# Optimization experiments

Hardware: AMD Instinct MI355X
Metric: run time of the kernel (lower is better)

Reference implementation:

```python
import jax, jax.numpy as jnp
import numpy as np

D_MODEL = 1024
N_HEADS = 16
HEAD_DIM = 64  # 'hidden' per head; n_heads*hidden == d_model


def setup_inputs() -> dict:
    key = jax.random.key(0)
    ks = jax.random.split(key, 11)
    B, S = 4, 2048
    scale = 1.0 / np.sqrt(D_MODEL)
    return {
        "query": jax.random.normal(ks[0], (B, S, D_MODEL), jnp.float32),
        "key": jax.random.normal(ks[1], (B, S, D_MODEL), jnp.float32),
        "value": jax.random.normal(ks[2], (B, S, D_MODEL), jnp.float32),
        "Wq": jax.random.normal(ks[3], (D_MODEL, N_HEADS * HEAD_DIM), jnp.float32) * scale,
        "bq": jnp.zeros((N_HEADS * HEAD_DIM,), jnp.float32),
        "Wk": jax.random.normal(ks[4], (D_MODEL, N_HEADS * HEAD_DIM), jnp.float32) * scale,
        "bk": jnp.zeros((N_HEADS * HEAD_DIM,), jnp.float32),
        "Wv": jax.random.normal(ks[5], (D_MODEL, N_HEADS * HEAD_DIM), jnp.float32) * scale,
        "bv": jnp.zeros((N_HEADS * HEAD_DIM,), jnp.float32),
        "Wo": jax.random.normal(ks[6], (N_HEADS * HEAD_DIM, D_MODEL), jnp.float32) * scale,
        "bo": jnp.zeros((D_MODEL,), jnp.float32),
    }


def reference(query, key, value, Wq, bq, Wk, bk, Wv, bv, Wo, bo):
    B, Sq, _ = query.shape
    Sk = key.shape[1]
    # QKV projections -> [B, H, S, d]
    q = (query @ Wq + bq).reshape(B, Sq, N_HEADS, HEAD_DIM).transpose(0, 2, 1, 3)
    k = (key @ Wk + bk).reshape(B, Sk, N_HEADS, HEAD_DIM).transpose(0, 2, 1, 3)
    v = (value @ Wv + bv).reshape(B, Sk, N_HEADS, HEAD_DIM).transpose(0, 2, 1, 3)
    # scores [B, H, Sq, Sk]
    scores = jnp.einsum("bhqd,bhkd->bhqk", q, k) / np.sqrt(HEAD_DIM).astype(np.float32)
    probs = jax.nn.softmax(scores, axis=-1)  # dropout: identity (eval mode)
    z = jnp.einsum("bhqk,bhkd->bhqd", probs, v)
    z = z.transpose(0, 2, 1, 3).reshape(B, Sq, N_HEADS * HEAD_DIM)
    return z @ Wo + bo
```

## Files before the change

kernel.cpp:

```cpp
#include <hip/hip_runtime.h>
#include <hip/hip_bf16.h>

typedef unsigned short ushort_t;
typedef unsigned int u32;
typedef __attribute__((ext_vector_type(8))) short short8;
typedef short8 __attribute__((may_alias)) short8_ma;
typedef __attribute__((ext_vector_type(4))) float f32x4;
typedef f32x4 __attribute__((may_alias)) f32x4_ma;
typedef __attribute__((ext_vector_type(2))) unsigned int u32x2;
typedef u32x2 __attribute__((may_alias)) u32x2_ma;
typedef __attribute__((ext_vector_type(4))) unsigned int u32x4;
typedef u32x4 __attribute__((may_alias)) u32x4_ma;

#if __has_builtin(__builtin_amdgcn_exp2f)
#define EXP2(x) __builtin_amdgcn_exp2f(x)
#else
#define EXP2(x) exp2f(x)
#endif

__device__ __forceinline__ unsigned short f2bf(float f) {
    union { float f; unsigned int i; } x; x.f = f;
    unsigned int r = x.i + 0x7FFFu + ((x.i >> 16) & 1u);
    return (unsigned short)(r >> 16);
}
__device__ __forceinline__ unsigned int bfround(float f) {
    union { float f; unsigned int i; } x; x.f = f;
    return x.i + 0x7FFFu + ((x.i >> 16) & 1u);
}
__device__ __forceinline__ unsigned int pack2bf(float lo, float hi) {
    return __builtin_amdgcn_perm(bfround(hi), bfround(lo), 0x07060302u);
}
__device__ __forceinline__ u32 cvtpk_bf16(float lo, float hi) {
    u32 r;
    asm("v_cvt_pk_bf16_f32 %0, %1, %2" : "=v"(r) : "v"(lo), "v"(hi));
    return r;
}
__device__ __forceinline__ f32x4 mfma16x16x32(short8 a, short8 b, f32x4 c) {
    return __builtin_amdgcn_mfma_f32_16x16x32_bf16(a, b, c, 0, 0, 0);
}
typedef const __attribute__((address_space(1))) u32 gu32;
typedef __attribute__((address_space(3))) u32 lu32;
__device__ __forceinline__ void async16(const ushort_t* g, ushort_t* l) {
    __builtin_amdgcn_global_load_lds((gu32*)g, (lu32*)l, 16, 0, 0);
}

__global__ __launch_bounds__(256)
void cast3(const float* __restrict__ A0, const float* __restrict__ A1,
           const float* __restrict__ A2, ushort_t* __restrict__ O0,
           ushort_t* __restrict__ O1, ushort_t* __restrict__ O2) {
    const float* A; ushort_t* O;
    switch (blockIdx.z) {
        case 0: A = A0; O = O0; break;
        case 1: A = A1; O = O1; break;
        default: A = A2; O = O2; break;
    }
    size_t idx = ((size_t)blockIdx.x * 256 + threadIdx.x) * 8;
    f32x4 v0 = *(const f32x4_ma*)(A + idx);
    f32x4 v1 = *(const f32x4_ma*)(A + idx + 4);
    u32x4 pk;
    pk[0] = pack2bf(v0[0], v0[1]);
    pk[1] = pack2bf(v0[2], v0[3]);
    pk[2] = pack2bf(v1[0], v1[1]);
    pk[3] = pack2bf(v1[2], v1[3]);
    *(u32x4_ma*)(O + idx) = pk;
}

__global__ __launch_bounds__(256)
void transpose4(const float* __restrict__ W0, const float* __restrict__ W1,
                const float* __restrict__ W2, const float* __restrict__ W3,
                ushort_t* __restrict__ T0, ushort_t* __restrict__ T1,
                ushort_t* __restrict__ T2, ushort_t* __restrict__ T3) {
    __shared__ ushort_t tile[64][65];
    const float* W; ushort_t* T;
    switch (blockIdx.z) {
        case 0: W = W0; T = T0; break;
        case 1: W = W1; T = T1; break;
        case 2: W = W2; T = T2; break;
        default: W = W3; T = T3; break;
    }
    int bx = blockIdx.x * 64, by = blockIdx.y * 64;
    int tx = threadIdx.x & 63, ty = threadIdx.x >> 6;
    #pragma unroll
    for (int i = 0; i < 64; i += 4)
        tile[ty + i][tx] = f2bf(W[(size_t)(by + ty + i) * 1024 + bx + tx]);
    __syncthreads();
    #pragma unroll
    for (int i = 0; i < 64; i += 4)
        T[(size_t)(bx + ty + i) * 1024 + by + tx] = tile[tx][ty + i];
}

template<int MODE>
__global__ __launch_bounds__(256)
void gemm_async(const ushort_t* __restrict__ A, const ushort_t* __restrict__ Bt,
                const float* __restrict__ bias, void* __restrict__ Cab,
                int M, int N, int K, float outscale) {
    __shared__ __align__(16) ushort_t As[2][128 * 64];
    __shared__ __align__(16) ushort_t Bs[2][128 * 64];
    const int t = threadIdx.x;
    const int old = blockIdx.x + (blockIdx.y << 3);
    const int neu = ((old & 7) << 6) | (old >> 3);
    const int n0 = (neu & 7) * 128, m0 = (neu >> 3) * 128;
    const int w = t >> 6, lane = t & 63, quad = lane >> 4, lr = lane & 15;
    const int wm = (w >> 1) * 64, wn = (w & 1) * 64;
    const int lrow8 = lane >> 3, lchunk = lane & 7;
    const int sw = (lchunk ^ lrow8) * 8;

    f32x4 acc[4][4] = {};

    #define STAGEAB(dst, koff) do { \
        _Pragma("unroll") \
        for (int i_ = 0; i_ < 4; i_++) { \
            int ra_ = 32 * w + 8 * i_ + lrow8; \
            async16(A  + (size_t)(m0 + ra_) * K + (koff) + sw, &As[dst][(32 * w + 8 * i_) * 64]); \
            async16(Bt + (size_t)(n0 + ra_) * K + (koff) + sw, &Bs[dst][(32 * w + 8 * i_) * 64]); \
        } } while (0)

    STAGEAB(0, 0);

    int cur = 0;
    for (int k0 = 0; k0 < K; k0 += 64) {
        __syncthreads();
        if (k0 + 64 < K)
            STAGEAB(cur ^ 1, k0 + 64);
        #pragma unroll
        for (int kc = 0; kc < 2; kc++) {
            short8 af[4], bf[4];
            int pa = ((4 * kc + quad) ^ (lr & 7)) * 8;
            #pragma unroll
            for (int i = 0; i < 4; i++) {
                af[i] = *(const short8_ma*)(As[cur] + (wm + i * 16 + lr) * 64 + pa);
                bf[i] = *(const short8_ma*)(Bs[cur] + (wn + i * 16 + lr) * 64 + pa);
            }
            #pragma unroll
            for (int i = 0; i < 4; i++)
                #pragma unroll
                for (int j = 0; j < 4; j++)
                    acc[i][j] = mfma16x16x32(af[i], bf[j], acc[i][j]);
        }
        cur ^= 1;
    }
    #undef STAGEAB

    #pragma unroll
    for (int i = 0; i < 4; i++) {
        int row = m0 + wm + i * 16 + quad * 4;
        #pragma unroll
        for (int j = 0; j < 4; j++) {
            int col = n0 + wn + j * 16 + lr;
            float bv = bias[col];
            if (MODE == 2) {
                u32x2 pw;
                pw[0] = cvtpk_bf16(acc[i][j][0] + bv, acc[i][j][1] + bv);
                pw[1] = cvtpk_bf16(acc[i][j][2] + bv, acc[i][j][3] + bv);
                size_t vrow = (size_t)(((row >> 11) << 4) | (col >> 6)) * 64 + (col & 63);
                *(u32x2_ma*)((ushort_t*)Cab + vrow * 2048 + (row & 2047)) = pw;
            } else {
                #pragma unroll
                for (int r = 0; r < 4; r++) {
                    size_t idx = (size_t)(row + r) * N + col;
                    if (MODE == 1) ((float*)Cab)[idx] = acc[i][j][r] + bv;
                    else ((ushort_t*)Cab)[idx] = f2bf((acc[i][j][r] + bv) * outscale);
                }
            }
        }
    }
}

__global__ __launch_bounds__(256)
void attn_fwd(const ushort_t* __restrict__ Q, const ushort_t* __restrict__ Kg,
              const ushort_t* __restrict__ VtG, ushort_t* __restrict__ Z) {
    __shared__ __align__(16) ushort_t Ks[2][64 * 64];
    __shared__ __align__(16) ushort_t Vt[2][64 * 64];
    __shared__ __align__(16) ushort_t Pt[128 * 64];

    const int t = threadIdx.x;
    const int old = blockIdx.x + (blockIdx.y << 4);
    const int neu = ((old & 7) << 7) | (old >> 3);
    const int qt = neu & 15;
    const int bh = neu >> 4;
    const int b = bh >> 4, h = bh & 15;
    const int w = t >> 6, lane = t & 63, quad = lane >> 4, lr = lane & 15;
    const int lrow8 = lane >> 3, lchunk = lane & 7;

    const size_t rs = 1024;
    const size_t qbase = ((size_t)b * 2048 + qt * 128) * rs + h * 64;
    const size_t kvbase = ((size_t)b * 2048) * rs + h * 64;
    const size_t vbase = (size_t)bh * 64 * 2048;

    short8 qf[2][2];
    #pragma unroll
    for (int mt = 0; mt < 2; mt++)
        #pragma unroll
        for (int kc = 0; kc < 2; kc++)
            qf[mt][kc] = *(const short8_ma*)(Q + qbase + (size_t)(w * 32 + mt * 16 + lr) * rs + kc * 32 + quad * 8);

    f32x4 oacc[2][4] = {};
    float lsum[2] = { 0.f, 0.f };

    const int rloc0 = 16 * w + lrow8;
    const int sw = (lchunk ^ lrow8) * 8;

    #pragma unroll
    for (int i = 0; i < 2; i++) {
        int rloc = rloc0 + 8 * i;
        async16(Kg + kvbase + (size_t)rloc * rs + sw, &Ks[0][(16 * w + 8 * i) * 64]);
        async16(VtG + vbase + (size_t)rloc * 2048 + sw, &Vt[0][(16 * w + 8 * i) * 64]);
    }

    int cur = 0;
    for (int kt = 0; kt < 32; kt++) {
        __syncthreads();
        if (kt < 31) {
            int nxt = cur ^ 1;
            #pragma unroll
            for (int i = 0; i < 2; i++) {
                int rloc = rloc0 + 8 * i;
                async16(Kg + kvbase + (size_t)((kt + 1) * 64 + rloc) * rs + sw, &Ks[nxt][(16 * w + 8 * i) * 64]);
                async16(VtG + vbase + (size_t)rloc * 2048 + (kt + 1) * 64 + sw, &Vt[nxt][(16 * w + 8 * i) * 64]);
            }
        }
        const ushort_t* Kc = Ks[cur];
        const ushort_t* Vc = Vt[cur];

        f32x4 sacc[4][2] = {};
        #pragma unroll
        for (int kc = 0; kc < 2; kc++) {
            short8 kf[4];
            int pa = ((4 * kc + quad) ^ (lr & 7)) * 8;
            #pragma unroll
            for (int nt = 0; nt < 4; nt++)
                kf[nt] = *(const short8_ma*)(Kc + (nt * 16 + lr) * 64 + pa);
            #pragma unroll
            for (int nt = 0; nt < 4; nt++)
                #pragma unroll
                for (int mt = 0; mt < 2; mt++)
                    sacc[nt][mt] = mfma16x16x32(kf[nt], qf[mt][kc], sacc[nt][mt]);
        }

        #pragma unroll
        for (int mt = 0; mt < 2; mt++) {
            const int prow = w * 32 + mt * 16 + lr;
            #pragma unroll
            for (int nt = 0; nt < 4; nt++) {
                float p0 = EXP2(sacc[nt][mt][0]);
                float p1 = EXP2(sacc[nt][mt][1]);
                float p2 = EXP2(sacc[nt][mt][2]);
                float p3 = EXP2(sacc[nt][mt][3]);
                lsum[mt] += (p0 + p1) + (p2 + p3);
                u32x2 pw;
                pw[0] = cvtpk_bf16(p0, p1);
                pw[1] = cvtpk_bf16(p2, p3);
                int phys = (2 * nt + (quad >> 1)) ^ (lr & 7);
                *(u32x2_ma*)(Pt + prow * 64 + phys * 8 + (quad & 1) * 4) = pw;
            }
        }

        asm volatile("" ::: "memory");

        #pragma unroll
        for (int kc2 = 0; kc2 < 2; kc2++) {
            short8 pf[2], vf[4];
            int pp = ((4 * kc2 + quad) ^ (lr & 7)) * 8;
            #pragma unroll
            for (int mt = 0; mt < 2; mt++)
                pf[mt] = *(const short8_ma*)(Pt + (w * 32 + mt * 16 + lr) * 64 + pp);
            #pragma unroll
            for (int dn = 0; dn < 4; dn++)
                vf[dn] = *(const short8_ma*)(Vc + (dn * 16 + lr) * 64 + pp);
            #pragma unroll
            for (int mt = 0; mt < 2; mt++)
                #pragma unroll
                for (int dn = 0; dn < 4; dn++)
                    oacc[mt][dn] = mfma16x16x32(vf[dn], pf[mt], oacc[mt][dn]);
        }
        cur ^= 1;
    }

    #pragma unroll
    for (int mt = 0; mt < 2; mt++) {
        lsum[mt] += __shfl_xor(lsum[mt], 16, 64);
        lsum[mt] += __shfl_xor(lsum[mt], 32, 64);
    }
    ushort_t* Ot = Pt;
    float inv[2] = { 1.f / lsum[0], 1.f / lsum[1] };
    asm volatile("" ::: "memory");
    #pragma unroll
    for (int mt = 0; mt < 2; mt++)
        #pragma unroll
        for (int dn = 0; dn < 4; dn++) {
            u32x2 pw;
            pw[0] = cvtpk_bf16(oacc[mt][dn][0] * inv[mt], oacc[mt][dn][1] * inv[mt]);
            pw[1] = cvtpk_bf16(oacc[mt][dn][2] * inv[mt], oacc[mt][dn][3] * inv[mt]);
            int phys = (2 * dn + (quad >> 1)) ^ (lr & 7);
            *(u32x2_ma*)(Ot + (w * 32 + mt * 16 + lr) * 64 + phys * 8 + (quad & 1) * 4) = pw;
        }
    asm volatile("" ::: "memory");
    {
        int qrow = t >> 1;
        int dhalf = (t & 1) * 32;
        #pragma unroll
        for (int cc = 0; cc < 4; cc++) {
            int phys = ((4 * (t & 1) + cc) ^ (qrow & 7)) * 8;
            short8 v = *(const short8_ma*)(Ot + qrow * 64 + phys);
            *(short8_ma*)(Z + qbase + (size_t)qrow * rs + dhalf + cc * 8) = v;
        }
    }
}

extern "C" void kernel_launch(void* const* d_in, const int* in_sizes, int n_in,
                              void* d_out, int out_size, void* d_ws, size_t ws_size,
                              hipStream_t stream) {
    const float* query = (const float*)d_in[0];
    const float* key   = (const float*)d_in[1];
    const float* value = (const float*)d_in[2];
    const float* Wq = (const float*)d_in[3];
    const float* bq = (const float*)d_in[4];
    const float* Wk = (const float*)d_in[5];
    const float* bk = (const float*)d_in[6];
    const float* Wv = (const float*)d_in[7];
    const float* bv = (const float*)d_in[8];
    const float* Wo = (const float*)d_in[9];
    const float* bo = (const float*)d_in[10];
    float* out = (float*)d_out;

    char* ws = (char*)d_ws;
    const size_t WSZ = 1024ull * 1024 * 2;
    const size_t QSZ = 8192ull * 1024 * 2;
    const size_t BW = 4 * WSZ;
    ushort_t* WqT = (ushort_t*)(ws + 0 * WSZ);
    ushort_t* WkT = (ushort_t*)(ws + 1 * WSZ);
    ushort_t* WvT = (ushort_t*)(ws + 2 * WSZ);
    ushort_t* WoT = (ushort_t*)(ws + 3 * WSZ);
    ushort_t* S1 = (ushort_t*)(ws + BW + 0 * QSZ);
    ushort_t* S2 = (ushort_t*)(ws + BW + 1 * QSZ);
    ushort_t* S3 = (ushort_t*)(ws + BW + 2 * QSZ);
    ushort_t* S4 = (ushort_t*)(ws + BW + 3 * QSZ);

    cast3<<<dim3(4096, 1, 3), 256, 0, stream>>>(query, key, value, S1, S2, S3);
    transpose4<<<dim3(16, 16, 4), 256, 0, stream>>>(Wq, Wk, Wv, Wo, WqT, WkT, WvT, WoT);

    dim3 gg(8, 64);
    gemm_async<0><<<gg, 256, 0, stream>>>(S1, WqT, bq, S4, 8192, 1024, 1024, 0.125f * 1.4426950408889634f);
    gemm_async<0><<<gg, 256, 0, stream>>>(S2, WkT, bk, S1, 8192, 1024, 1024, 1.0f);
    gemm_async<2><<<gg, 256, 0, stream>>>(S3, WvT, bv, S2, 8192, 1024, 1024, 1.0f);

    attn_fwd<<<dim3(16, 64), 256, 0, stream>>>(S4, S1, S2, S4);

    gemm_async<1><<<gg, 256, 0, stream>>>(S4, WoT, bo, out, 8192, 1024, 1024, 1.0f);
}
```

Baseline: 349.6 us.

## Load K and V fragments directly from global memory in attention loop

Removes the double-buffered shared-memory staging of K and V tiles and the per-iteration block barrier. Each wave now reads its K and V MFMA fragments straight from global memory (relying on L1/L2) and issues the V loads early to overlap with the softmax. This removes LDS traffic and synchronisation, but each of the four waves now fetches the same K/V data redundantly from global memory, and there is no explicit prefetch of the next tile.

```diff
diff --git a/kernel.cpp b/kernel.cpp
--- a/kernel.cpp
+++ b/kernel.cpp
@@ -169,8 +169,6 @@
 __global__ __launch_bounds__(256)
 void attn_fwd(const ushort_t* __restrict__ Q, const ushort_t* __restrict__ Kg,
               const ushort_t* __restrict__ VtG, ushort_t* __restrict__ Z) {
-    __shared__ __align__(16) ushort_t Ks[2][64 * 64];
-    __shared__ __align__(16) ushort_t Vt[2][64 * 64];
     __shared__ __align__(16) ushort_t Pt[128 * 64];
 
     const int t = threadIdx.x;
@@ -180,7 +178,6 @@
     const int bh = neu >> 4;
     const int b = bh >> 4, h = bh & 15;
     const int w = t >> 6, lane = t & 63, quad = lane >> 4, lr = lane & 15;
-    const int lrow8 = lane >> 3, lchunk = lane & 7;
 
     const size_t rs = 1024;
     const size_t qbase = ((size_t)b * 2048 + qt * 128) * rs + h * 64;
@@ -197,45 +194,30 @@
     f32x4 oacc[2][4] = {};
     float lsum[2] = { 0.f, 0.f };
 
-    const int rloc0 = 16 * w + lrow8;
-    const int sw = (lchunk ^ lrow8) * 8;
-
-    #pragma unroll
-    for (int i = 0; i < 2; i++) {
-        int rloc = rloc0 + 8 * i;
-        async16(Kg + kvbase + (size_t)rloc * rs + sw, &Ks[0][(16 * w + 8 * i) * 64]);
-        async16(VtG + vbase + (size_t)rloc * 2048 + sw, &Vt[0][(16 * w + 8 * i) * 64]);
-    }
-
-    int cur = 0;
+    const ushort_t* kp = Kg + kvbase + (size_t)lr * rs + quad * 8;
+    const ushort_t* vp = VtG + vbase + (size_t)lr * 2048 + quad * 8;
+
     for (int kt = 0; kt < 32; kt++) {
-        __syncthreads();
-        if (kt < 31) {
-            int nxt = cur ^ 1;
-            #pragma unroll
-            for (int i = 0; i < 2; i++) {
-                int rloc = rloc0 + 8 * i;
-                async16(Kg + kvbase + (size_t)((kt + 1) * 64 + rloc) * rs + sw, &Ks[nxt][(16 * w + 8 * i) * 64]);
-                async16(VtG + vbase + (size_t)rloc * 2048 + (kt + 1) * 64 + sw, &Vt[nxt][(16 * w + 8 * i) * 64]);
-            }
-        }
-        const ushort_t* Kc = Ks[cur];
-        const ushort_t* Vc = Vt[cur];
-
         f32x4 sacc[4][2] = {};
         #pragma unroll
         for (int kc = 0; kc < 2; kc++) {
             short8 kf[4];
-            int pa = ((4 * kc + quad) ^ (lr & 7)) * 8;
             #pragma unroll
             for (int nt = 0; nt < 4; nt++)
-                kf[nt] = *(const short8_ma*)(Kc + (nt * 16 + lr) * 64 + pa);
+                kf[nt] = *(const short8_ma*)(kp + (size_t)(kt * 64 + nt * 16) * rs + kc * 32);
             #pragma unroll
             for (int nt = 0; nt < 4; nt++)
                 #pragma unroll
                 for (int mt = 0; mt < 2; mt++)
                     sacc[nt][mt] = mfma16x16x32(kf[nt], qf[mt][kc], sacc[nt][mt]);
         }
+
+        short8 vf[2][4];
+        #pragma unroll
+        for (int kc2 = 0; kc2 < 2; kc2++)
+            #pragma unroll
+            for (int dn = 0; dn < 4; dn++)
+                vf[kc2][dn] = *(const short8_ma*)(vp + (size_t)(dn * 16) * 2048 + kt * 64 + kc2 * 32);
 
         #pragma unroll
         for (int mt = 0; mt < 2; mt++) {
@@ -259,21 +241,18 @@
 
         #pragma unroll
         for (int kc2 = 0; kc2 < 2; kc2++) {
-            short8 pf[2], vf[4];
+            short8 pf[2];
             int pp = ((4 * kc2 + quad) ^ (lr & 7)) * 8;
             #pragma unroll
             for (int mt = 0; mt < 2; mt++)
                 pf[mt] = *(const short8_ma*)(Pt + (w * 32 + mt * 16 + lr) * 64 + pp);
-            #pragma unroll
-            for (int dn = 0; dn < 4; dn++)
-                vf[dn] = *(const short8_ma*)(Vc + (dn * 16 + lr) * 64 + pp);
             #pragma unroll
             for (int mt = 0; mt < 2; mt++)
                 #pragma unroll
                 for (int dn = 0; dn < 4; dn++)
-                    oacc[mt][dn] = mfma16x16x32(vf[dn], pf[mt], oacc[mt][dn]);
-        }
-        cur ^= 1;
+                    oacc[mt][dn] = mfma16x16x32(vf[kc2][dn], pf[mt], oacc[mt][dn]);
+        }
+        asm volatile("" ::: "memory");
     }
 
     #pragma unroll
```

Result: slower. 529.4 us (+51.4%).

## Double wavefronts per block in GEMM and attention kernels

Applied to the files above, without the earlier changes.

Both the projection GEMM and the attention kernel move from 256 to 512 threads per block, keeping the same 128x128 and 128-query tiles. Each wavefront now owns half as many output rows (32x64 in the GEMM, 16 query rows in attention), and the async staging loads, fragment loads and epilogue writes are redistributed to match. The goal is more wavefronts in flight to hide memory and MFMA latency, with fewer registers per wave. The cost is that each wave reuses fewer B/K/V fragments per LDS read and barriers span more waves.

```diff
diff --git a/kernel.cpp b/kernel.cpp
--- a/kernel.cpp
+++ b/kernel.cpp
@@ -90,7 +90,7 @@
 }
 
 template<int MODE>
-__global__ __launch_bounds__(256)
+__global__ __launch_bounds__(512)
 void gemm_async(const ushort_t* __restrict__ A, const ushort_t* __restrict__ Bt,
                 const float* __restrict__ bias, void* __restrict__ Cab,
                 int M, int N, int K, float outscale) {
@@ -101,18 +101,18 @@
     const int neu = ((old & 7) << 6) | (old >> 3);
     const int n0 = (neu & 7) * 128, m0 = (neu >> 3) * 128;
     const int w = t >> 6, lane = t & 63, quad = lane >> 4, lr = lane & 15;
-    const int wm = (w >> 1) * 64, wn = (w & 1) * 64;
+    const int wm = (w & 3) * 32, wn = (w >> 2) * 64;
     const int lrow8 = lane >> 3, lchunk = lane & 7;
     const int sw = (lchunk ^ lrow8) * 8;
 
-    f32x4 acc[4][4] = {};
+    f32x4 acc[2][4] = {};
 
     #define STAGEAB(dst, koff) do { \
         _Pragma("unroll") \
-        for (int i_ = 0; i_ < 4; i_++) { \
-            int ra_ = 32 * w + 8 * i_ + lrow8; \
-            async16(A  + (size_t)(m0 + ra_) * K + (koff) + sw, &As[dst][(32 * w + 8 * i_) * 64]); \
-            async16(Bt + (size_t)(n0 + ra_) * K + (koff) + sw, &Bs[dst][(32 * w + 8 * i_) * 64]); \
+        for (int i_ = 0; i_ < 2; i_++) { \
+            int ra_ = 16 * w + 8 * i_ + lrow8; \
+            async16(A  + (size_t)(m0 + ra_) * K + (koff) + sw, &As[dst][(16 * w + 8 * i_) * 64]); \
+            async16(Bt + (size_t)(n0 + ra_) * K + (koff) + sw, &Bs[dst][(16 * w + 8 * i_) * 64]); \
         } } while (0)
 
     STAGEAB(0, 0);
@@ -124,15 +124,16 @@
             STAGEAB(cur ^ 1, k0 + 64);
         #pragma unroll
         for (int kc = 0; kc < 2; kc++) {
-            short8 af[4], bf[4];
+            short8 af[2], bf[4];
             int pa = ((4 * kc + quad) ^ (lr & 7)) * 8;
             #pragma unroll
-            for (int i = 0; i < 4; i++) {
+            for (int i = 0; i < 2; i++)
                 af[i] = *(const short8_ma*)(As[cur] + (wm + i * 16 + lr) * 64 + pa);
-                bf[i] = *(const short8_ma*)(Bs[cur] + (wn + i * 16 + lr) * 64 + pa);
-            }
-            #pragma unroll
-            for (int i = 0; i < 4; i++)
+            #pragma unroll
+            for (int j = 0; j < 4; j++)
+                bf[j] = *(const short8_ma*)(Bs[cur] + (wn + j * 16 + lr) * 64 + pa);
+            #pragma unroll
+            for (int i = 0; i < 2; i++)
                 #pragma unroll
                 for (int j = 0; j < 4; j++)
                     acc[i][j] = mfma16x16x32(af[i], bf[j], acc[i][j]);
@@ -142,7 +143,7 @@
     #undef STAGEAB
 
     #pragma unroll
-    for (int i = 0; i < 4; i++) {
+    for (int i = 0; i < 2; i++) {
         int row = m0 + wm + i * 16 + quad * 4;
         #pragma unroll
         for (int j = 0; j < 4; j++) {
@@ -166,7 +167,7 @@
     }
 }
 
-__global__ __launch_bounds__(256)
+__global__ __launch_bounds__(512)
 void attn_fwd(const ushort_t* __restrict__ Q, const ushort_t* __restrict__ Kg,
               const ushort_t* __restrict__ VtG, ushort_t* __restrict__ Z) {
     __shared__ __align__(16) ushort_t Ks[2][64 * 64];
@@ -187,42 +188,32 @@
     const size_t kvbase = ((size_t)b * 2048) * rs + h * 64;
     const size_t vbase = (size_t)bh * 64 * 2048;
 
-    short8 qf[2][2];
-    #pragma unroll
-    for (int mt = 0; mt < 2; mt++)
-        #pragma unroll
-        for (int kc = 0; kc < 2; kc++)
-            qf[mt][kc] = *(const short8_ma*)(Q + qbase + (size_t)(w * 32 + mt * 16 + lr) * rs + kc * 32 + quad * 8);
-
-    f32x4 oacc[2][4] = {};
-    float lsum[2] = { 0.f, 0.f };
-
-    const int rloc0 = 16 * w + lrow8;
+    short8 qf[2];
+    #pragma unroll
+    for (int kc = 0; kc < 2; kc++)
+        qf[kc] = *(const short8_ma*)(Q + qbase + (size_t)(w * 16 + lr) * rs + kc * 32 + quad * 8);
+
+    f32x4 oacc[4] = {};
+    float lsum = 0.f;
+
+    const int rloc0 = 8 * w + lrow8;
     const int sw = (lchunk ^ lrow8) * 8;
 
-    #pragma unroll
-    for (int i = 0; i < 2; i++) {
-        int rloc = rloc0 + 8 * i;
-        async16(Kg + kvbase + (size_t)rloc * rs + sw, &Ks[0][(16 * w + 8 * i) * 64]);
-        async16(VtG + vbase + (size_t)rloc * 2048 + sw, &Vt[0][(16 * w + 8 * i) * 64]);
-    }
+    async16(Kg + kvbase + (size_t)rloc0 * rs + sw, &Ks[0][(8 * w) * 64]);
+    async16(VtG + vbase + (size_t)rloc0 * 2048 + sw, &Vt[0][(8 * w) * 64]);
 
     int cur = 0;
     for (int kt = 0; kt < 32; kt++) {
         __syncthreads();
         if (kt < 31) {
             int nxt = cur ^ 1;
-            #pragma unroll
-            for (int i = 0; i < 2; i++) {
-                int rloc = rloc0 + 8 * i;
-                async16(Kg + kvbase + (size_t)((kt + 1) * 64 + rloc) * rs + sw, &Ks[nxt][(16 * w + 8 * i) * 64]);
-                async16(VtG + vbase + (size_t)rloc * 2048 + (kt + 1) * 64 + sw, &Vt[nxt][(16 * w + 8 * i) * 64]);
-            }
+            async16(Kg + kvbase + (size_t)((kt + 1) * 64 + rloc0) * rs + sw, &Ks[nxt][(8 * w) * 64]);
+            async16(VtG + vbase + (size_t)rloc0 * 2048 + (kt + 1) * 64 + sw, &Vt[nxt][(8 * w) * 64]);
         }
         const ushort_t* Kc = Ks[cur];
         const ushort_t* Vc = Vt[cur];
 
-        f32x4 sacc[4][2] = {};
+        f32x4 sacc[4] = {};
         #pragma unroll
         for (int kc = 0; kc < 2; kc++) {
             short8 kf[4];
@@ -232,21 +223,18 @@
                 kf[nt] = *(const short8_ma*)(Kc + (nt * 16 + lr) * 64 + pa);
             #pragma unroll
             for (int nt = 0; nt < 4; nt++)
-                #pragma unroll
-                for (int mt = 0; mt < 2; mt++)
-                    sacc[nt][mt] = mfma16x16x32(kf[nt], qf[mt][kc], sacc[nt][mt]);
-        }
-
-        #pragma unroll
-        for (int mt = 0; mt < 2; mt++) {
-            const int prow = w * 32 + mt * 16 + lr;
+                sacc[nt] = mfma16x16x32(kf[nt], qf[kc], sacc[nt]);
+        }
+
+        {
+            const int prow = w * 16 + lr;
             #pragma unroll
             for (int nt = 0; nt < 4; nt++) {
-                float p0 = EXP2(sacc[nt][mt][0]);
-                float p1 = EXP2(sacc[nt][mt][1]);
-                float p2 = EXP2(sacc[nt][mt][2]);
-                float p3 = EXP2(sacc[nt][mt][3]);
-                lsum[mt] += (p0 + p1) + (p2 + p3);
+                float p0 = EXP2(sacc[nt][0]);
+                float p1 = EXP2(sacc[nt][1]);
+                float p2 = EXP2(sacc[nt][2]);
+                float p3 = EXP2(sacc[nt][3]);
+                lsum += (p0 + p1) + (p2 + p3);
                 u32x2 pw;
                 pw[0] = cvtpk_bf16(p0, p1);
                 pw[1] = cvtpk_bf16(p2, p3);
@@ -259,50 +247,40 @@
 
         #pragma unroll
         for (int kc2 = 0; kc2 < 2; kc2++) {
-            short8 pf[2], vf[4];
             int pp = ((4 * kc2 + quad) ^ (lr & 7)) * 8;
-            #pragma unroll
-            for (int mt = 0; mt < 2; mt++)
-                pf[mt] = *(const short8_ma*)(Pt + (w * 32 + mt * 16 + lr) * 64 + pp);
-            #pragma unroll
-            for (int dn = 0; dn < 4; dn++)
-                vf[dn] = *(const short8_ma*)(Vc + (dn * 16 + lr) * 64 + pp);
-            #pragma unroll
-            for (int mt = 0; mt < 2; mt++)
-                #pragma unroll
-                for (int dn = 0; dn < 4; dn++)
-                    oacc[mt][dn] = mfma16x16x32(vf[dn], pf[mt], oacc[mt][dn]);
-        }
+            short8 pf = *(const short8_ma*)(Pt + (w * 16 + lr) * 64 + pp);
+            #pragma unroll
+            for (int dn = 0; dn < 4; dn++) {
+                short8 vf = *(const short8_ma*)(Vc + (dn * 16 + lr) * 64 + pp);
+                oacc[dn] = mfma16x16x32(vf, pf, oacc[dn]);
+            }
+        }
+        asm volatile("" ::: "memory");
         cur ^= 1;
     }
 
-    #pragma unroll
-    for (int mt = 0; mt < 2; mt++) {
-        lsum[mt] += __shfl_xor(lsum[mt], 16, 64);
-        lsum[mt] += __shfl_xor(lsum[mt], 32, 64);
-    }
+    lsum += __shfl_xor(lsum, 16, 64);
+    lsum += __shfl_xor(lsum, 32, 64);
     ushort_t* Ot = Pt;
-    float inv[2] = { 1.f / lsum[0], 1.f / lsum[1] };
+    float inv = 1.f / lsum;
     asm volatile("" ::: "memory");
     #pragma unroll
-    for (int mt = 0; mt < 2; mt++)
-        #pragma unroll
-        for (int dn = 0; dn < 4; dn++) {
-            u32x2 pw;
-            pw[0] = cvtpk_bf16(oacc[mt][dn][0] * inv[mt], oacc[mt][dn][1] * inv[mt]);
-            pw[1] = cvtpk_bf16(oacc[mt][dn][2] * inv[mt], oacc[mt][dn][3] * inv[mt]);
-            int phys = (2 * dn + (quad >> 1)) ^ (lr & 7);
-            *(u32x2_ma*)(Ot + (w * 32 + mt * 16 + lr) * 64 + phys * 8 + (quad & 1) * 4) = pw;
-        }
+    for (int dn = 0; dn < 4; dn++) {
+        u32x2 pw;
+        pw[0] = cvtpk_bf16(oacc[dn][0] * inv, oacc[dn][1] * inv);
+        pw[1] = cvtpk_bf16(oacc[dn][2] * inv, oacc[dn][3] * inv);
+        int phys = (2 * dn + (quad >> 1)) ^ (lr & 7);
+        *(u32x2_ma*)(Ot + (w * 16 + lr) * 64 + phys * 8 + (quad & 1) * 4) = pw;
+    }
     asm volatile("" ::: "memory");
     {
-        int qrow = t >> 1;
-        int dhalf = (t & 1) * 32;
-        #pragma unroll
-        for (int cc = 0; cc < 4; cc++) {
-            int phys = ((4 * (t & 1) + cc) ^ (qrow & 7)) * 8;
+        int qrow = t >> 2;
+        #pragma unroll
+        for (int cc = 0; cc < 2; cc++) {
+            int c2 = (t & 3) * 2 + cc;
+            int phys = (c2 ^ (qrow & 7)) * 8;
             short8 v = *(const short8_ma*)(Ot + qrow * 64 + phys);
-            *(short8_ma*)(Z + qbase + (size_t)qrow * rs + dhalf + cc * 8) = v;
+            *(short8_ma*)(Z + qbase + (size_t)qrow * rs + c2 * 8) = v;
         }
     }
 }
@@ -340,11 +318,11 @@
     transpose4<<<dim3(16, 16, 4), 256, 0, stream>>>(Wq, Wk, Wv, Wo, WqT, WkT, WvT, WoT);
 
     dim3 gg(8, 64);
-    gemm_async<0><<<gg, 256, 0, stream>>>(S1, WqT, bq, S4, 8192, 1024, 1024, 0.125f * 1.4426950408889634f);
-    gemm_async<0><<<gg, 256, 0, stream>>>(S2, WkT, bk, S1, 8192, 1024, 1024, 1.0f);
-    gemm_async<2><<<gg, 256, 0, stream>>>(S3, WvT, bv, S2, 8192, 1024, 1024, 1.0f);
-
-    attn_fwd<<<dim3(16, 64), 256, 0, stream>>>(S4, S1, S2, S4);
-
-    gemm_async<1><<<gg, 256, 0, stream>>>(S4, WoT, bo, out, 8192, 1024, 1024, 1.0f);
-}
+    gemm_async<0><<<gg, 512, 0, stream>>>(S1, WqT, bq, S4, 8192, 1024, 1024, 0.125f * 1.4426950408889634f);
+    gemm_async<0><<<gg, 512, 0, stream>>>(S2, WkT, bk, S1, 8192, 1024, 1024, 1.0f);
+    gemm_async<2><<<gg, 512, 0, stream>>>(S3, WvT, bv, S2, 8192, 1024, 1024, 1.0f);
+
+    attn_fwd<<<dim3(16, 64), 512, 0, stream>>>(S4, S1, S2, S4);
+
+    gemm_async<1><<<gg, 512, 0, stream>>>(S4, WoT, bo, out, 8192, 1024, 1024, 1.0f);
+}
```

Result: no change. 344.0 us (-1.6%).
